# Optimization experiments

Measured on AMD Instinct MI355X. Metric: run time of the kernel, lower is better.

Reference implementation:

```python
import jax, jax.numpy as jnp
import numpy as np

NEG_INF = -1e10  # masked_fill value from the torch module


def setup_inputs() -> dict:
    key = jax.random.key(0)
    k1, k2, k3, k4, k5 = jax.random.split(key, 5)
    B, S, H = 64, 2048, 512
    return {
        "decoder_hidden": jax.random.normal(k1, (B, H), dtype=jnp.float32),
        "encoder_outputs": jax.random.normal(k2, (B, S, 2 * H), dtype=jnp.float32),
        "mask": jnp.ones((B, S), dtype=jnp.int32),
        "Wd": jax.random.normal(k3, (H, H), dtype=jnp.float32) * (1.0 / np.sqrt(H)),
        "We": jax.random.normal(k4, (2 * H, H), dtype=jnp.float32) * (1.0 / np.sqrt(2 * H)),
        "v": jax.random.normal(k5, (H,), dtype=jnp.float32) * (1.0 / np.sqrt(H)),
    }


def reference(decoder_hidden, encoder_outputs, mask, Wd, We, v):
    # decoder_proj: (B, H); encoder_proj: (B, S, H)
    dec_proj = decoder_hidden @ Wd
    enc_proj = jnp.einsum("bse,eh->bsh", encoder_outputs, We)
    energy = jnp.tanh(dec_proj[:, None, :] + enc_proj)  # (B, S, H)
    scores = jnp.einsum("bsh,h->bs", energy, v)  # (B, S)
    scores = jnp.where(mask == 0, NEG_INF, scores)
    attn_weights = jax.nn.softmax(scores, axis=1)  # (B, S)
    context = jnp.einsum("bs,bsd->bd", attn_weights, encoder_outputs)  # (B, 2H)
    return (context, attn_weights)
```

## Files before the change

### kernel.cpp

```cpp
#include <hip/hip_runtime.h>

typedef _Float16 f16;
typedef f16  f16x4 __attribute__((ext_vector_type(4)));
typedef f16  f16x8 __attribute__((ext_vector_type(8)));
typedef float f32x4 __attribute__((ext_vector_type(4)));

#define B_  64
#define S_  2048
#define H_  512
#define K_  1024

__device__ __forceinline__ float fast_tanh(float x){
  float ax = fabsf(x);
  float t  = __expf(-2.0f*ax);
  float r  = (1.0f - t) / (1.0f + t);
  return x < 0.0f ? -r : r;
}

__global__ __launch_bounds__(256) void prep_k(const float* __restrict__ We,
                                              f16* __restrict__ Bg,
                                              const float* __restrict__ dh,
                                              const float* __restrict__ Wd,
                                              float* __restrict__ dp,
                                              const float* __restrict__ vvg,
                                              float* __restrict__ vC){
  __shared__ float s_dh[512];
  if (blockIdx.x < 2048){
    int idx = blockIdx.x*256 + threadIdx.x;
    int k = idx >> 9, col = idx & 511;
    Bg[((k>>3)<<12) + (col<<3) + (k&7)] = (f16)We[idx];
  } else if (blockIdx.x < 2176){
    int idx = blockIdx.x - 2048;
    int b = idx >> 1, cg = idx & 1;
    int col = (cg<<8) + threadIdx.x;
    for (int i = threadIdx.x; i < 512; i += 256) s_dh[i] = dh[(b<<9) + i];
    __syncthreads();
    float a0=0.f,a1=0.f,a2=0.f,a3=0.f;
    for (int k = 0; k < 512; k += 4){
      a0 += s_dh[k+0]*Wd[(k+0)*512 + col];
      a1 += s_dh[k+1]*Wd[(k+1)*512 + col];
      a2 += s_dh[k+2]*Wd[(k+2)*512 + col];
      a3 += s_dh[k+3]*Wd[(k+3)*512 + col];
    }
    dp[(b<<9) + col] = (a0+a1)+(a2+a3);
  } else {
    int t = threadIdx.x;
    float a = fabsf(vvg[t]) + fabsf(vvg[t+256]);
    #pragma unroll
    for (int o = 32; o >= 1; o >>= 1) a += __shfl_xor(a, o);
    if ((t & 63) == 0) s_dh[t>>6] = a;
    __syncthreads();
    if (t == 0) vC[0] = s_dh[0]+s_dh[1]+s_dh[2]+s_dh[3];
  }
}

__global__ __launch_bounds__(512, 2) void fused_k(
    const float* __restrict__ enc,
    const f16*   __restrict__ Bg,
    const float* __restrict__ dp,
    const float* __restrict__ vvg,
    const float* __restrict__ vC,
    const int*   __restrict__ mask,
    float*       __restrict__ pbuf,
    float*       __restrict__ denom,
    float*       __restrict__ part)
{
  __shared__ __align__(16) f16 At[2][2048];
  __shared__ float s_sc[64];

  const int tid  = threadIdx.x;
  const int lane = tid & 63;
  const int wave = tid >> 6;
  const int b    = blockIdx.x >> 5;
  const int s0   = (blockIdx.x & 31) << 6;

  if (tid < 64) s_sc[tid] = 0.0f;

  const int arow = tid >> 3;
  const int akq  = tid & 7;
  const int kgrp = akq >> 1, apar = akq & 1;
  const float* aG = enc + ((size_t)(b*S_ + s0 + arow) << 10) + (akq << 2);
  const int aDst = (kgrp<<9) + ((arow ^ (kgrp<<1))<<3) + (apar<<2);

  const int r16 = lane & 15, g = lane >> 4;
  const int aFrag = (g<<9) + ((r16 ^ (g<<1))<<3);
  const int colb  = wave << 6;

  const f16* bP = Bg + (g<<12) + ((colb + r16)<<3);

  f32x4 acc[4][4] = {};

  auto loadA = [&](int t)->f32x4 { return *(const f32x4*)(aG + (t<<5)); };
  auto putA  = [&](f32x4 a4, int buf){
    f16x4 h4; h4[0]=(f16)a4[0]; h4[1]=(f16)a4[1]; h4[2]=(f16)a4[2]; h4[3]=(f16)a4[3];
    *(f16x4*)&At[buf][aDst] = h4;
  };

  {
    f32x4 a0 = loadA(0);
    putA(a0, 0);
  }
  f32x4 aCur = loadA(1);
  asm volatile("s_waitcnt lgkmcnt(0)" ::: "memory");
  __builtin_amdgcn_sched_barrier(0);
  __builtin_amdgcn_s_barrier();
  __builtin_amdgcn_sched_barrier(0);

  for (int t = 0; t < 32; ++t){
    const int cur = t & 1;
    f32x4 aNext;
    if (t < 31){
      putA(aCur, cur^1);
    }
    f16x8 bfr[4];
    #pragma unroll
    for (int n = 0; n < 4; ++n)
      bfr[n] = *(const f16x8*)(bP + (n<<7));
    if (t < 31){
      aNext = loadA(t+2 <= 31 ? t+2 : 31);
    }
    __builtin_amdgcn_s_setprio(1);
    #pragma unroll
    for (int m = 0; m < 4; ++m){
      f16x8 af = *(const f16x8*)&At[cur][aFrag + (m<<7)];
      #pragma unroll
      for (int n = 0; n < 4; ++n)
        acc[m][n] = __builtin_amdgcn_mfma_f32_16x16x32_f16(af, bfr[n], acc[m][n], 0, 0, 0);
    }
    __builtin_amdgcn_s_setprio(0);
    if (t < 31){
      asm volatile("s_waitcnt lgkmcnt(0)" ::: "memory");
      __builtin_amdgcn_sched_barrier(0);
      __builtin_amdgcn_s_barrier();
      __builtin_amdgcn_sched_barrier(0);
      aCur = aNext;
    }
    bP += (1<<14);
  }

  float dpv[4], vvv[4];
  #pragma unroll
  for (int n = 0; n < 4; ++n){
    int c = colb + (n<<4) + r16;
    dpv[n] = dp[(b<<9) + c];
    vvv[n] = vvg[c];
  }
  float sp[4][4];
  #pragma unroll
  for (int m = 0; m < 4; ++m)
    #pragma unroll
    for (int r = 0; r < 4; ++r) sp[m][r] = 0.f;
  #pragma unroll
  for (int m = 0; m < 4; ++m)
    #pragma unroll
    for (int n = 0; n < 4; ++n)
      #pragma unroll
      for (int r = 0; r < 4; ++r){
        float e = fast_tanh(acc[m][n][r] + dpv[n]);
        sp[m][r] += vvv[n]*e;
      }
  #pragma unroll
  for (int m = 0; m < 4; ++m)
    #pragma unroll
    for (int r = 0; r < 4; ++r){
      float x = sp[m][r];
      x += __shfl_xor(x, 1);
      x += __shfl_xor(x, 2);
      x += __shfl_xor(x, 4);
      x += __shfl_xor(x, 8);
      if (r16 == 0) atomicAdd(&s_sc[(m<<4) + (g<<2) + r], x);
    }
  __syncthreads();

  const float C = vC[0];
  if (tid < 64){
    float s = s_sc[tid];
    int mk = mask[(b<<11) + s0 + tid];
    float p = mk ? __expf(s - C) : 0.0f;
    s_sc[tid] = p;
    pbuf[(b<<11) + s0 + tid] = p;
    float d = p;
    #pragma unroll
    for (int o = 32; o >= 1; o >>= 1) d += __shfl_xor(d, o);
    if (tid == 0) denom[(b<<5) + (blockIdx.x & 31)] = d;
  }
  __syncthreads();

  {
    const float2* e2 = (const float2*)(enc + ((size_t)(b*S_ + s0) << 10)) + tid;
    float ax = 0.f, ay = 0.f;
    #pragma unroll 4
    for (int s = 0; s < 64; ++s){
      float w = s_sc[s];
      float2 x = e2[s*512];
      ax += w * x.x; ay += w * x.y;
    }
    float2* pp = (float2*)part + ((size_t)blockIdx.x << 9) + tid;
    *pp = make_float2(ax, ay);
  }
}

__global__ __launch_bounds__(256) void combine_k(const float* __restrict__ part,
                                                 const float* __restrict__ denom,
                                                 const float* __restrict__ pbuf,
                                                 float* __restrict__ ctx,
                                                 float* __restrict__ attn){
  const int b = blockIdx.x, tid = threadIdx.x;
  float D = 0.f;
  #pragma unroll
  for (int c = 0; c < 32; ++c) D += denom[(b<<5) + c];
  D = fmaxf(D, 1e-37f);
  const float inv = 1.0f / D;

  f32x4 acc = {0.f,0.f,0.f,0.f};
  const f32x4* p4 = (const f32x4*)part;
  #pragma unroll
  for (int c = 0; c < 32; ++c)
    acc += p4[(((b<<5)+c)<<8) + tid];
  ((f32x4*)ctx)[(b<<8) + tid] = acc * inv;

  #pragma unroll
  for (int i = 0; i < 8; ++i){
    int s = tid + (i<<8);
    attn[(b<<11) + s] = pbuf[(b<<11) + s] * inv;
  }
}

extern "C" void kernel_launch(void* const* d_in, const int* in_sizes, int n_in,
                              void* d_out, int out_size, void* d_ws, size_t ws_size,
                              hipStream_t stream){
  (void)in_sizes; (void)n_in; (void)out_size;
  const size_t WS_NEED = 1712384u + 8388608u;
  if (ws_size < WS_NEED) return;

  const float* dec_h = (const float*)d_in[0];
  const float* enc   = (const float*)d_in[1];
  const int*   mask  = (const int*)d_in[2];
  const float* Wd    = (const float*)d_in[3];
  const float* We    = (const float*)d_in[4];
  const float* v     = (const float*)d_in[5];
  float* out  = (float*)d_out;
  float* ctx  = out;
  float* attn = out + B_*2*H_;

  char* ws = (char*)d_ws;
  f16*   Bg     = (f16*)ws;
  float* dproj  = (float*)(ws + 1048576);
  float* vC     = (float*)(ws + 1179648);
  float* pbuf   = (float*)(ws + 1179904);
  float* denom  = (float*)(ws + 1704192);
  float* part   = (float*)(ws + 1712384);

  prep_k   <<<2177, 256, 0, stream>>>(We, Bg, dec_h, Wd, dproj, v, vC);
  fused_k  <<<2048, 512, 0, stream>>>(enc, Bg, dproj, v, vC, mask, pbuf, denom, part);
  combine_k<<<B_, 256, 0, stream>>>(part, denom, pbuf, ctx, attn);
}
```

Baseline: 288.0 us.

## Widen A-tile K-step to 128 to cut barriers and widen global loads

The GEMM main loop now stages a 64x128 f16 A tile per iteration instead of 64x32, so there are 8 iterations with 4 inner MFMA sub-steps each rather than 32 iterations. Each thread loads 64 contiguous bytes of encoder data per step and writes two 16-byte LDS chunks using a new XOR swizzle. This cuts the number of block-wide barriers and issues fewer, larger global loads per thread, so more data is in flight. The cost is four times the LDS (32 KB for the double buffer) and more live registers, which may hurt the two-blocks-per-CU occupancy target.

```diff
diff --git a/kernel.cpp b/kernel.cpp
--- a/kernel.cpp
+++ b/kernel.cpp
@@ -65,7 +65,7 @@
     float*       __restrict__ denom,
     float*       __restrict__ part)
 {
-  __shared__ __align__(16) f16 At[2][2048];
+  __shared__ __align__(16) f16 At[2][8192];
   __shared__ float s_sc[64];
 
   const int tid  = threadIdx.x;
@@ -77,65 +77,79 @@
   if (tid < 64) s_sc[tid] = 0.0f;
 
   const int arow = tid >> 3;
-  const int akq  = tid & 7;
-  const int kgrp = akq >> 1, apar = akq & 1;
-  const float* aG = enc + ((size_t)(b*S_ + s0 + arow) << 10) + (akq << 2);
-  const int aDst = (kgrp<<9) + ((arow ^ (kgrp<<1))<<3) + (apar<<2);
+  const int ac   = tid & 7;
+  const float* aG = enc + ((size_t)(b*S_ + s0 + arow) << 10) + (ac << 4);
+  const int kg0   = ac << 1;
+  const int aDst0 = (kg0<<9)     + ((arow ^ (kg0&7))<<3);
+  const int aDst1 = ((kg0+1)<<9) + ((arow ^ ((kg0+1)&7))<<3);
 
   const int r16 = lane & 15, g = lane >> 4;
-  const int aFrag = (g<<9) + ((r16 ^ (g<<1))<<3);
   const int colb  = wave << 6;
-
-  const f16* bP = Bg + (g<<12) + ((colb + r16)<<3);
+  const f16* bS = Bg + ((size_t)(colb + r16) << 3);
 
   f32x4 acc[4][4] = {};
 
-  auto loadA = [&](int t)->f32x4 { return *(const f32x4*)(aG + (t<<5)); };
-  auto putA  = [&](f32x4 a4, int buf){
-    f16x4 h4; h4[0]=(f16)a4[0]; h4[1]=(f16)a4[1]; h4[2]=(f16)a4[2]; h4[3]=(f16)a4[3];
-    *(f16x4*)&At[buf][aDst] = h4;
+  struct A16 { f32x4 q0, q1, q2, q3; };
+  auto loadA = [&](int T)->A16 {
+    const float* p = aG + (T<<7);
+    A16 r;
+    r.q0 = *(const f32x4*)(p);
+    r.q1 = *(const f32x4*)(p+4);
+    r.q2 = *(const f32x4*)(p+8);
+    r.q3 = *(const f32x4*)(p+12);
+    return r;
   };
-
+  auto putA = [&](const A16& a, int buf){
+    f16x8 lo, hi;
+    lo[0]=(f16)a.q0[0]; lo[1]=(f16)a.q0[1]; lo[2]=(f16)a.q0[2]; lo[3]=(f16)a.q0[3];
+    lo[4]=(f16)a.q1[0]; lo[5]=(f16)a.q1[1]; lo[6]=(f16)a.q1[2]; lo[7]=(f16)a.q1[3];
+    hi[0]=(f16)a.q2[0]; hi[1]=(f16)a.q2[1]; hi[2]=(f16)a.q2[2]; hi[3]=(f16)a.q2[3];
+    hi[4]=(f16)a.q3[0]; hi[5]=(f16)a.q3[1]; hi[6]=(f16)a.q3[2]; hi[7]=(f16)a.q3[3];
+    *(f16x8*)&At[buf][aDst0] = lo;
+    *(f16x8*)&At[buf][aDst1] = hi;
+  };
+
+  A16 aHold;
   {
-    f32x4 a0 = loadA(0);
+    A16 a0 = loadA(0);
+    aHold  = loadA(1);
     putA(a0, 0);
   }
-  f32x4 aCur = loadA(1);
   asm volatile("s_waitcnt lgkmcnt(0)" ::: "memory");
   __builtin_amdgcn_sched_barrier(0);
   __builtin_amdgcn_s_barrier();
   __builtin_amdgcn_sched_barrier(0);
 
-  for (int t = 0; t < 32; ++t){
-    const int cur = t & 1;
-    f32x4 aNext;
-    if (t < 31){
-      putA(aCur, cur^1);
-    }
-    f16x8 bfr[4];
-    #pragma unroll
-    for (int n = 0; n < 4; ++n)
-      bfr[n] = *(const f16x8*)(bP + (n<<7));
-    if (t < 31){
-      aNext = loadA(t+2 <= 31 ? t+2 : 31);
-    }
-    __builtin_amdgcn_s_setprio(1);
-    #pragma unroll
-    for (int m = 0; m < 4; ++m){
-      f16x8 af = *(const f16x8*)&At[cur][aFrag + (m<<7)];
+  for (int T = 0; T < 8; ++T){
+    const int cur = T & 1;
+    if (T < 7) putA(aHold, cur^1);
+    #pragma unroll
+    for (int kk = 0; kk < 4; ++kk){
+      const int kgl = (kk<<2) + g;
+      const int kgG = (T<<4) + kgl;
+      f16x8 bfr[4];
       #pragma unroll
       for (int n = 0; n < 4; ++n)
-        acc[m][n] = __builtin_amdgcn_mfma_f32_16x16x32_f16(af, bfr[n], acc[m][n], 0, 0, 0);
-    }
-    __builtin_amdgcn_s_setprio(0);
-    if (t < 31){
+        bfr[n] = *(const f16x8*)(bS + ((size_t)kgG<<12) + (n<<7));
+      f16x8 af[4];
+      #pragma unroll
+      for (int m = 0; m < 4; ++m)
+        af[m] = *(const f16x8*)&At[cur][(kgl<<9) + ((((m<<4)+r16) ^ (kgl&7))<<3)];
+      __builtin_amdgcn_s_setprio(1);
+      #pragma unroll
+      for (int m = 0; m < 4; ++m)
+        #pragma unroll
+        for (int n = 0; n < 4; ++n)
+          acc[m][n] = __builtin_amdgcn_mfma_f32_16x16x32_f16(af[m], bfr[n], acc[m][n], 0, 0, 0);
+      __builtin_amdgcn_s_setprio(0);
+    }
+    if (T < 6) aHold = loadA(T+2);
+    if (T < 7){
       asm volatile("s_waitcnt lgkmcnt(0)" ::: "memory");
       __builtin_amdgcn_sched_barrier(0);
       __builtin_amdgcn_s_barrier();
       __builtin_amdgcn_sched_barrier(0);
-      aCur = aNext;
-    }
-    bP += (1<<14);
+    }
   }
 
   float dpv[4], vvv[4];
```

Measured after the change: 324.7 us. 1.13x slower.
